# Kernel optimization log

Hardware: AMD Instinct MI355X
Metric: run time of the kernel (lower is better)

The kernel has to match this reference:

```python
import jax, jax.numpy as jnp
import numpy as np

B, S, D, H = 2, 2048, 1024, 16
HD = D // H
EPS = 1e-5


def layer_norm(x, g, b):
    m = jnp.mean(x, axis=-1, keepdims=True)
    v = jnp.mean(jnp.square(x - m), axis=-1, keepdims=True)
    return (x - m) * jax.lax.rsqrt(v + EPS) * g + b


def setup_inputs() -> dict:
    key = jax.random.key(0)
    ks = jax.random.split(key, 16)
    s = 0.02
    x = jax.random.normal(ks[0], (B, S, D), dtype=jnp.float32)
    mask = jax.random.randint(ks[1], (1, 1, S, S), 0, 2, dtype=jnp.int32)
    return {
        "x": x,
        "mask": mask,
        "Wq": jax.random.normal(ks[2], (D, D), jnp.float32) * s,
        "Wk": jax.random.normal(ks[3], (D, D), jnp.float32) * s,
        "Wv": jax.random.normal(ks[4], (D, D), jnp.float32) * s,
        "Wo": jax.random.normal(ks[5], (D, D), jnp.float32) * s,
        "bo": jax.random.normal(ks[6], (D,), jnp.float32) * s,
        "ln1_g": jnp.ones((D,), jnp.float32),
        "ln1_b": jnp.zeros((D,), jnp.float32),
        "W1": jax.random.normal(ks[7], (D, 4 * D), jnp.float32) * s,
        "b1": jax.random.normal(ks[8], (4 * D,), jnp.float32) * s,
        "W2": jax.random.normal(ks[9], (4 * D, D), jnp.float32) * s,
        "b2": jax.random.normal(ks[10], (D,), jnp.float32) * s,
        "ln2_g": jnp.ones((D,), jnp.float32),
        "ln2_b": jnp.zeros((D,), jnp.float32),
    }


def reference(x, mask, Wq, Wk, Wv, Wo, bo, ln1_g, ln1_b, W1, b1, W2, b2, ln2_g, ln2_b):
    # --- multi-head attention (dropout = identity in eval) ---
    q = (x @ Wq).reshape(B, S, H, HD)
    k = (x @ Wk).reshape(B, S, H, HD)
    v = (x @ Wv).reshape(B, S, H, HD)
    scores = jnp.einsum("bshd,bthd->bhst", q, k) / jnp.sqrt(jnp.float32(HD))
    scores = jnp.where(mask == 1, jnp.float32(-1e9), scores)
    p = jax.nn.softmax(scores, axis=-1)
    o = jnp.einsum("bhst,bthd->bshd", p, v).reshape(B, S, D)
    attn_out = o @ Wo + bo
    # --- residual with norm on the branch (note: norm applied to attn output) ---
    x = x + layer_norm(attn_out, ln1_g, ln1_b)
    # --- FFN: gelu after fc1 AND after fc2 (as in source) ---
    h = jax.nn.gelu(x @ W1 + b1, approximate=False)
    h = jax.nn.gelu(h @ W2 + b2, approximate=False)
    x = x + layer_norm(h, ln2_g, ln2_b)
    return x
```

## Files before the change

kernel.cpp:

```cpp
#include <hip/hip_runtime.h>
#include <hip/hip_bf16.h>
#include <cstdint>

#define BB 2
#define SS 2048
#define DD 1024
#define HH 16
#define HDIM 64
#define MROWS (BB*SS)

typedef __bf16 bf16;
using bf16x8 = __bf16 __attribute__((ext_vector_type(8)));
using bf16x4 = __bf16 __attribute__((ext_vector_type(4)));
using bf16x2 = __bf16 __attribute__((ext_vector_type(2)));
using f32x4  = float __attribute__((ext_vector_type(4)));

__device__ __forceinline__ float gelu_exact(float x) {
    return 0.5f * x * (1.f + erff(x * 0.70710678118654752f));
}

__device__ __forceinline__ void stage16(const bf16* g, bf16* lds_chunk_base, int lane) {
#if __has_builtin(__builtin_amdgcn_global_load_lds)
    __builtin_amdgcn_global_load_lds((const __attribute__((address_space(1))) void*)g,
                                     (__attribute__((address_space(3))) void*)lds_chunk_base,
                                     16, 0, 0);
#else
    *(bf16x8*)(lds_chunk_base + lane * 8) = *(const bf16x8*)g;
#endif
}

__global__ __launch_bounds__(256) void prep_kernel(
    const float* __restrict__ x, bf16* __restrict__ x_b,
    const int* __restrict__ mask, unsigned long long* __restrict__ maskb,
    const float* __restrict__ Wq, const float* __restrict__ Wk,
    const float* __restrict__ Wv, const float* __restrict__ Wo,
    const float* __restrict__ W1, const float* __restrict__ W2,
    bf16* __restrict__ Wqkv_t, bf16* __restrict__ Wo_t,
    bf16* __restrict__ W1_t, bf16* __restrict__ W2_t) {
    const int bid = blockIdx.x;
    if (bid < 4096) {
        int i = bid * 256 + threadIdx.x;
        float4 v = ((const float4*)x)[i];
        bf16x4 o;
        o[0] = (bf16)v.x; o[1] = (bf16)v.y; o[2] = (bf16)v.z; o[3] = (bf16)v.w;
        *(bf16x4*)(x_b + (size_t)i * 4) = o;
        return;
    }
    if (bid < 20480) {
        int gid = (bid - 4096) * 256 + threadIdx.x;
        int mv = mask[gid];
        unsigned long long bal = __ballot(mv == 1);
        if ((threadIdx.x & 63) == 0) maskb[gid >> 6] = bal;
        return;
    }
    int t = bid - 20480;
    const float* W; bf16* Wt; int K, N, bx, by;
    if (t < 4096) {
        int wsel = t >> 10;
        int tt = t & 1023;
        W  = (wsel == 0) ? Wq : (wsel == 1) ? Wk : (wsel == 2) ? Wv : Wo;
        Wt = (wsel == 3) ? Wo_t : (Wqkv_t + (size_t)wsel * 1024 * 1024);
        K = 1024; N = 1024; bx = (tt & 31) * 32; by = (tt >> 5) * 32;
    } else if (t < 8192) {
        int tt = t - 4096;
        W = W1; Wt = W1_t; K = 1024; N = 4096;
        bx = (tt & 127) * 32; by = (tt >> 7) * 32;
    } else {
        int tt = t - 8192;
        W = W2; Wt = W2_t; K = 4096; N = 1024;
        bx = (tt & 31) * 32; by = (tt >> 5) * 32;
    }
    __shared__ float tile[32][33];
    int tx = threadIdx.x & 31;
    int ty = threadIdx.x >> 5;
#pragma unroll
    for (int j = 0; j < 4; ++j)
        tile[ty + j * 8][tx] = W[(size_t)(by + ty + j * 8) * N + bx + tx];
    __syncthreads();
#pragma unroll
    for (int j = 0; j < 4; ++j)
        Wt[(size_t)(bx + ty + j * 8) * K + by + tx] = (bf16)tile[tx][ty + j * 8];
}

template <int EPI>
__global__ __launch_bounds__(256, 3) void gemm_bt(const bf16* __restrict__ A,
                                                  const bf16* __restrict__ Bt,
                                                  void* __restrict__ C,
                                                  void* __restrict__ C2,
                                                  const float* __restrict__ bias,
                                                  int M, int N, int K, int ldk) {
    __shared__ __align__(16) bf16 As[128 * 64];
    __shared__ __align__(16) bf16 Bs[128 * 64];
    const int tid  = threadIdx.x;
    const int lane = tid & 63;
    const int wave = tid >> 6;
    const int l16  = lane & 15;
    const int quad = lane >> 4;
    const int wm = wave >> 1, wn = wave & 1;
    const int m0 = blockIdx.y * 128, n0 = blockIdx.x * 128;
    const int z  = blockIdx.z;
    A  += (size_t)z * K;
    Bt += (size_t)z * K;

    f32x4 acc[4][4];
#pragma unroll
    for (int i = 0; i < 4; ++i)
#pragma unroll
        for (int j = 0; j < 4; ++j) acc[i][j] = (f32x4){0.f, 0.f, 0.f, 0.f};

    const int nsteps = K >> 6;
    for (int kt = 0; kt < nsteps; ++kt) {
        const int kbase = kt << 6;
#pragma unroll
        for (int c = 0; c < 4; ++c) {
            int chunk = wave * 4 + c;
            int gi = chunk * 64 + lane;
            int m  = gi >> 3;
            int cp = gi & 7;
            int g  = cp ^ (m & 7);
            stage16(A  + (size_t)(m0 + m) * ldk + kbase + g * 8, As + chunk * 512, lane);
            stage16(Bt + (size_t)(n0 + m) * ldk + kbase + g * 8, Bs + chunk * 512, lane);
        }
        __syncthreads();
#pragma unroll
        for (int ks = 0; ks < 2; ++ks) {
            bf16x8 af[4], bfr[4];
#pragma unroll
            for (int i = 0; i < 4; ++i) {
                int m = wm * 64 + i * 16 + l16;
                int g = ks * 4 + quad;
                af[i]  = *(const bf16x8*)(As + m * 64 + ((g ^ (m & 7)) * 8));
                int n = wn * 64 + i * 16 + l16;
                bfr[i] = *(const bf16x8*)(Bs + n * 64 + ((g ^ (n & 7)) * 8));
            }
#pragma unroll
            for (int i = 0; i < 4; ++i)
#pragma unroll
                for (int j = 0; j < 4; ++j)
                    acc[i][j] = __builtin_amdgcn_mfma_f32_16x16x32_bf16(af[i], bfr[j], acc[i][j], 0, 0, 0);
        }
        __syncthreads();
    }

    float* Cz = (EPI == 4) ? (z ? (float*)C2 : (float*)C) : nullptr;
#pragma unroll
    for (int i = 0; i < 4; ++i) {
        int row = m0 + wm * 64 + i * 16 + quad * 4;
#pragma unroll
        for (int j = 0; j < 4; ++j) {
            int col = n0 + wn * 64 + j * 16 + l16;
            float bv = (EPI == 2) ? bias[col] : 0.f;
#pragma unroll
            for (int r = 0; r < 4; ++r) {
                float v = acc[i][j][r];
                if (EPI == 2) v = gelu_exact(v + bv);
                size_t idx = (size_t)(row + r) * N + col;
                if (EPI == 4) Cz[idx] = v;
                else          ((bf16*)C)[idx] = (bf16)v;
            }
        }
    }
}

template <int EPI>
__global__ __launch_bounds__(512, 2) void gemm256(const bf16* __restrict__ A,
                                                  const bf16* __restrict__ Bt,
                                                  void* __restrict__ C0, void* __restrict__ C1,
                                                  void* __restrict__ C2v, void* __restrict__ C3,
                                                  const float* __restrict__ bias,
                                                  int M, int N, int K, int ldk) {
    __shared__ __align__(16) bf16 As[2 * 256 * 64];
    __shared__ __align__(16) bf16 Bs[2 * 256 * 64];
    const int tid  = threadIdx.x;
    const int lane = tid & 63;
    const int wave = tid >> 6;
    const int l16  = lane & 15;
    const int quad = lane >> 4;
    const int wm = wave >> 2;
    const int wn = wave & 3;
    const int m0 = blockIdx.y * 256, n0 = blockIdx.x * 256;
    const int z  = blockIdx.z;
    A  += (size_t)z * K;
    Bt += (size_t)z * K;

    const int rl = lane >> 3;
    const int cpn = lane & 7;
    const bf16* pA[4]; const bf16* pB[4];
    int ldsoff[4];
#pragma unroll
    for (int c = 0; c < 4; ++c) {
        int row = wave * 32 + c * 8 + rl;
        int g = cpn ^ (row & 7);
        pA[c] = A + (size_t)(m0 + row) * ldk + g * 8;
        pB[c] = Bt + (size_t)(n0 + row) * ldk + g * 8;
        ldsoff[c] = (wave * 4 + c) * 512;
    }

    f32x4 acc[8][4];
#pragma unroll
    for (int i = 0; i < 8; ++i)
#pragma unroll
        for (int j = 0; j < 4; ++j) acc[i][j] = (f32x4){0.f, 0.f, 0.f, 0.f};

    const int nt = K >> 6;

    auto stage_tile = [&](int t) {
        const int kb = t << 6;
        bf16* dstA = As + (t & 1) * 16384;
        bf16* dstB = Bs + (t & 1) * 16384;
#pragma unroll
        for (int c = 0; c < 4; ++c) stage16(pA[c] + kb, dstA + ldsoff[c], lane);
#pragma unroll
        for (int c = 0; c < 4; ++c) stage16(pB[c] + kb, dstB + ldsoff[c], lane);
    };

    stage_tile(0);
    stage_tile(1);
    asm volatile("s_waitcnt vmcnt(8)" ::: "memory");
    __builtin_amdgcn_s_barrier();

    for (int t = 0; t < nt; ++t) {
        const bf16* AsP = As + (t & 1) * 16384;
        const bf16* BsP = Bs + (t & 1) * 16384;
        bf16x8 af[4][2], b0[2][2], b1[2][2];

#pragma unroll
        for (int i = 0; i < 4; ++i) {
            int row = wm * 128 + i * 16 + l16;
#pragma unroll
            for (int kk = 0; kk < 2; ++kk)
                af[i][kk] = *(const bf16x8*)(AsP + row * 64 + (((kk * 4 + quad) ^ (row & 7)) * 8));
        }
#pragma unroll
        for (int j = 0; j < 2; ++j) {
            int row = wn * 64 + j * 16 + l16;
#pragma unroll
            for (int kk = 0; kk < 2; ++kk)
                b0[j][kk] = *(const bf16x8*)(BsP + row * 64 + (((kk * 4 + quad) ^ (row & 7)) * 8));
        }
        __builtin_amdgcn_s_barrier();
        __builtin_amdgcn_s_setprio(1);
#pragma unroll
        for (int i = 0; i < 4; ++i)
#pragma unroll
            for (int j = 0; j < 2; ++j)
#pragma unroll
                for (int kk = 0; kk < 2; ++kk)
                    acc[i][j] = __builtin_amdgcn_mfma_f32_16x16x32_bf16(af[i][kk], b0[j][kk], acc[i][j], 0, 0, 0);
        __builtin_amdgcn_s_setprio(0);
        __builtin_amdgcn_s_barrier();

#pragma unroll
        for (int j = 0; j < 2; ++j) {
            int row = wn * 64 + (j + 2) * 16 + l16;
#pragma unroll
            for (int kk = 0; kk < 2; ++kk)
                b1[j][kk] = *(const bf16x8*)(BsP + row * 64 + (((kk * 4 + quad) ^ (row & 7)) * 8));
        }
        __builtin_amdgcn_s_barrier();
        __builtin_amdgcn_s_setprio(1);
#pragma unroll
        for (int i = 0; i < 4; ++i)
#pragma unroll
            for (int j = 0; j < 2; ++j)
#pragma unroll
                for (int kk = 0; kk < 2; ++kk)
                    acc[i][j + 2] = __builtin_amdgcn_mfma_f32_16x16x32_bf16(af[i][kk], b1[j][kk], acc[i][j + 2], 0, 0, 0);
        __builtin_amdgcn_s_setprio(0);
        __builtin_amdgcn_s_barrier();

#pragma unroll
        for (int i = 0; i < 4; ++i) {
            int row = wm * 128 + 64 + i * 16 + l16;
#pragma unroll
            for (int kk = 0; kk < 2; ++kk)
                af[i][kk] = *(const bf16x8*)(AsP + row * 64 + (((kk * 4 + quad) ^ (row & 7)) * 8));
        }
        __builtin_amdgcn_s_barrier();
        __builtin_amdgcn_s_setprio(1);
#pragma unroll
        for (int i = 0; i < 4; ++i)
#pragma unroll
            for (int j = 0; j < 2; ++j)
#pragma unroll
                for (int kk = 0; kk < 2; ++kk)
                    acc[i + 4][j + 2] = __builtin_amdgcn_mfma_f32_16x16x32_bf16(af[i][kk], b1[j][kk], acc[i + 4][j + 2], 0, 0, 0);
        __builtin_amdgcn_s_setprio(0);
        __builtin_amdgcn_s_barrier();

        if (t + 2 < nt) stage_tile(t + 2);
        __builtin_amdgcn_s_barrier();
        __builtin_amdgcn_s_setprio(1);
#pragma unroll
        for (int i = 0; i < 4; ++i)
#pragma unroll
            for (int j = 0; j < 2; ++j)
#pragma unroll
                for (int kk = 0; kk < 2; ++kk)
                    acc[i + 4][j] = __builtin_amdgcn_mfma_f32_16x16x32_bf16(af[i][kk], b0[j][kk], acc[i + 4][j], 0, 0, 0);
        __builtin_amdgcn_s_setprio(0);
        if (t + 2 < nt) { asm volatile("s_waitcnt vmcnt(8)" ::: "memory"); }
        else            { asm volatile("s_waitcnt vmcnt(0)" ::: "memory"); }
        __builtin_amdgcn_s_barrier();
    }

    float* Cz = nullptr;
    if (EPI == 4) Cz = (z == 0) ? (float*)C0 : (z == 1) ? (float*)C1 : (z == 2) ? (float*)C2v : (float*)C3;
#pragma unroll
    for (int i = 0; i < 8; ++i) {
        int row = m0 + wm * 128 + i * 16 + quad * 4;
#pragma unroll
        for (int j = 0; j < 4; ++j) {
            int col = n0 + wn * 64 + j * 16 + l16;
            float bv = (EPI == 2) ? bias[col] : 0.f;
#pragma unroll
            for (int r = 0; r < 4; ++r) {
                float v = acc[i][j][r];
                if (EPI == 2) v = gelu_exact(v + bv);
                size_t idx = (size_t)(row + r) * N + col;
                if (EPI == 4) Cz[idx] = v;
                else          ((bf16*)C0)[idx] = (bf16)v;
            }
        }
    }
}

__global__ __launch_bounds__(512, 4) void flash_attn(const bf16* __restrict__ qkv,
                                                     const unsigned long long* __restrict__ maskb,
                                                     bf16* __restrict__ o) {
    __shared__ __align__(16) bf16 Ks[128 * 64];
    __shared__ __align__(16) bf16 Vts[64 * 136];
    const int tid  = threadIdx.x;
    const int lane = tid & 63;
    const int wave = tid >> 6;
    const int l16  = lane & 15;
    const int quad = lane >> 4;
    const int bh = blockIdx.y;
    const int b = bh >> 4, h = bh & 15;
    const int q0 = blockIdx.x * 128;
    const size_t rowb = (size_t)b * SS;
    const float SCL = 0.18033688011112042f;

    const size_t qrow = (rowb + q0 + wave * 16 + l16) * 3072 + h * 64;
    bf16x8 qf[2];
    {
        bf16x8 q0r = *(const bf16x8*)(qkv + qrow + quad * 8);
        bf16x8 q1r = *(const bf16x8*)(qkv + qrow + 32 + quad * 8);
#pragma unroll
        for (int j = 0; j < 8; ++j) {
            qf[0][j] = (bf16)((float)q0r[j] * SCL);
            qf[1][j] = (bf16)((float)q1r[j] * SCL);
        }
    }

    f32x4 oacc[4];
#pragma unroll
    for (int d = 0; d < 4; ++d) oacc[d] = (f32x4){0.f, 0.f, 0.f, 0.f};
    f32x4 lacc = (f32x4){0.f, 0.f, 0.f, 0.f};
    const int mrow32 = (q0 + wave * 16 + l16) * 32;

    bf16x8 ones;
#pragma unroll
    for (int j = 0; j < 8; ++j) ones[j] = (bf16)1.0f;

    const int vt_tc = (lane >> 4) * 32 + ((lane >> 1) & 3) * 8 + ((lane >> 3) & 1) * 4 + 2 * (lane & 1);
    const int vd8 = wave * 8;

    int kst[2], ksg[2];
#pragma unroll
    for (int c = 0; c < 2; ++c) {
        int gi = (wave * 2 + c) * 64 + lane;
        kst[c] = gi >> 3;
        ksg[c] = (gi & 7) ^ (kst[c] & 7);
    }

    bf16x8 kreg[2], vreg[2];
    ulonglong2 mwreg;
#pragma unroll
    for (int c = 0; c < 2; ++c)
        kreg[c] = *(const bf16x8*)(qkv + (rowb + kst[c]) * 3072 + 1024 + h * 64 + ksg[c] * 8);
    {
        const bf16* vg = qkv + (rowb + 2 * lane) * 3072 + 2048 + h * 64 + vd8;
        vreg[0] = *(const bf16x8*)(vg);
        vreg[1] = *(const bf16x8*)(vg + 3072);
    }
    mwreg = *(const ulonglong2*)(maskb + mrow32);

    for (int kt = 0; kt < SS / 128; ++kt) {
        __syncthreads();
#pragma unroll
        for (int c = 0; c < 2; ++c)
            *(bf16x8*)(Ks + (wave * 2 + c) * 512 + lane * 8) = kreg[c];
#pragma unroll
        for (int j = 0; j < 8; ++j) {
            bf16x2 pr; pr[0] = vreg[0][j]; pr[1] = vreg[1][j];
            *(bf16x2*)(Vts + (vd8 + j) * 136 + vt_tc) = pr;
        }
        ulonglong2 mw = mwreg;
        __syncthreads();

        if (kt + 1 < SS / 128) {
            const int t0n = (kt + 1) * 128;
#pragma unroll
            for (int c = 0; c < 2; ++c)
                kreg[c] = *(const bf16x8*)(qkv + (rowb + t0n + kst[c]) * 3072 + 1024 + h * 64 + ksg[c] * 8);
            {
                const bf16* vg = qkv + (rowb + t0n + 2 * lane) * 3072 + 2048 + h * 64 + vd8;
                vreg[0] = *(const bf16x8*)(vg);
                vreg[1] = *(const bf16x8*)(vg + 3072);
            }
            mwreg = *(const ulonglong2*)(maskb + mrow32 + (kt + 1) * 2);
        }

        f32x4 st[8];
        __builtin_amdgcn_s_setprio(1);
#pragma unroll
        for (int tg = 0; tg < 8; ++tg) {
            int tl = tg * 16 + l16;
            bf16x8 a0 = *(const bf16x8*)(Ks + tl * 64 + ((quad       ^ (tl & 7)) * 8));
            bf16x8 a1 = *(const bf16x8*)(Ks + tl * 64 + (((4 + quad) ^ (tl & 7)) * 8));
            f32x4 s = (f32x4){0.f, 0.f, 0.f, 0.f};
            s = __builtin_amdgcn_mfma_f32_16x16x32_bf16(a0, qf[0], s, 0, 0, 0);
            s = __builtin_amdgcn_mfma_f32_16x16x32_bf16(a1, qf[1], s, 0, 0, 0);
            st[tg] = s;
        }
        __builtin_amdgcn_s_setprio(0);

        unsigned long long s0 = mw.x >> (quad * 4);
        unsigned long long s1 = mw.y >> (quad * 4);
        bf16x8 pva[4];
#pragma unroll
        for (int tg = 0; tg < 8; ++tg) {
            unsigned int bits = (unsigned int)(((tg < 4) ? s0 : s1) >> ((tg & 3) * 16));
#pragma unroll
            for (int r = 0; r < 4; ++r) {
                float p = __builtin_amdgcn_exp2f(st[tg][r]);
                p = ((bits >> r) & 1u) ? 0.f : p;
                pva[tg >> 1][(tg & 1) * 4 + r] = (bf16)p;
            }
        }

        __builtin_amdgcn_s_setprio(1);
#pragma unroll
        for (int kc = 0; kc < 4; ++kc) {
#pragma unroll
            for (int dg = 0; dg < 4; ++dg) {
                bf16x8 bfrag = *(const bf16x8*)(Vts + (dg * 16 + l16) * 136 + kc * 32 + quad * 8);
                oacc[dg] = __builtin_amdgcn_mfma_f32_16x16x32_bf16(pva[kc], bfrag, oacc[dg], 0, 0, 0);
            }
            lacc = __builtin_amdgcn_mfma_f32_16x16x32_bf16(pva[kc], ones, lacc, 0, 0, 0);
        }
        __builtin_amdgcn_s_setprio(0);
    }

#pragma unroll
    for (int r = 0; r < 4; ++r) {
        float inv_l = 1.f / lacc[r];
        bf16* orow = o + (rowb + q0 + wave * 16 + quad * 4 + r) * DD + h * 64;
#pragma unroll
        for (int dg = 0; dg < 4; ++dg)
            orow[dg * 16 + l16] = (bf16)(oacc[dg][r] * inv_l);
    }
}

template <bool GELU, bool WB16, int NP>
__global__ __launch_bounds__(256) void ln_fused(const float* __restrict__ resid,
                                                const float* __restrict__ p0,
                                                const float* __restrict__ p1,
                                                const float* __restrict__ p2,
                                                const float* __restrict__ p3,
                                                const float* __restrict__ bias,
                                                const float* __restrict__ g,
                                                const float* __restrict__ bb,
                                                float* __restrict__ outf,
                                                bf16* __restrict__ outb) {
    const int row = blockIdx.x;
    const int tid = threadIdx.x;
    const size_t base = (size_t)row * DD + tid * 4;
    float4 a0 = *(const float4*)(p0 + base);
    float4 a1 = *(const float4*)(p1 + base);
    float4 bz = *(const float4*)(bias + tid * 4);
    float ax = a0.x + a1.x + bz.x;
    float ay = a0.y + a1.y + bz.y;
    float az = a0.z + a1.z + bz.z;
    float aw = a0.w + a1.w + bz.w;
    if (NP == 4) {
        float4 a2 = *(const float4*)(p2 + base);
        float4 a3 = *(const float4*)(p3 + base);
        ax += a2.x + a3.x; ay += a2.y + a3.y; az += a2.z + a3.z; aw += a2.w + a3.w;
    }
    if (GELU) { ax = gelu_exact(ax); ay = gelu_exact(ay); az = gelu_exact(az); aw = gelu_exact(aw); }
    float s1 = ax + ay + az + aw;
    float s2 = ax * ax + ay * ay + az * az + aw * aw;
#pragma unroll
    for (int off = 32; off; off >>= 1) {
        s1 += __shfl_xor(s1, off, 64);
        s2 += __shfl_xor(s2, off, 64);
    }
    __shared__ float red[8];
    if ((tid & 63) == 0) { red[(tid >> 6) * 2] = s1; red[(tid >> 6) * 2 + 1] = s2; }
    __syncthreads();
    s1 = red[0] + red[2] + red[4] + red[6];
    s2 = red[1] + red[3] + red[5] + red[7];
    float mean = s1 * (1.f / DD);
    float var  = s2 * (1.f / DD) - mean * mean;
    float rs = rsqrtf(var + 1e-5f);
    float4 gv = *(const float4*)(g + tid * 4);
    float4 bv = *(const float4*)(bb + tid * 4);
    float4 rv = *(const float4*)(resid + base);
    float y0 = rv.x + (ax - mean) * rs * gv.x + bv.x;
    float y1 = rv.y + (ay - mean) * rs * gv.y + bv.y;
    float y2 = rv.z + (az - mean) * rs * gv.z + bv.z;
    float y3 = rv.w + (aw - mean) * rs * gv.w + bv.w;
    float4 yo = make_float4(y0, y1, y2, y3);
    *(float4*)(outf + base) = yo;
    if (WB16) {
        bf16x4 ob;
        ob[0] = (bf16)y0; ob[1] = (bf16)y1; ob[2] = (bf16)y2; ob[3] = (bf16)y3;
        *(bf16x4*)(outb + base) = ob;
    }
}

extern "C" void kernel_launch(void* const* d_in, const int* in_sizes, int n_in,
                              void* d_out, int out_size, void* d_ws, size_t ws_size,
                              hipStream_t stream) {
    const float* x    = (const float*)d_in[0];
    const int*   mask = (const int*)d_in[1];
    const float* Wq   = (const float*)d_in[2];
    const float* Wk   = (const float*)d_in[3];
    const float* Wv   = (const float*)d_in[4];
    const float* Wo   = (const float*)d_in[5];
    const float* bo   = (const float*)d_in[6];
    const float* ln1g = (const float*)d_in[7];
    const float* ln1b = (const float*)d_in[8];
    const float* W1   = (const float*)d_in[9];
    const float* b1   = (const float*)d_in[10];
    const float* W2   = (const float*)d_in[11];
    const float* b2   = (const float*)d_in[12];
    const float* ln2g = (const float*)d_in[13];
    const float* ln2b = (const float*)d_in[14];

    char* w = (char*)d_ws;
    bf16* Wqkv_t = (bf16*)w; w += (size_t)3072 * 1024 * 2;
    bf16* Wo_t   = (bf16*)w; w += (size_t)1024 * 1024 * 2;
    bf16* W1_t   = (bf16*)w; w += (size_t)4096 * 1024 * 2;
    bf16* W2_t   = (bf16*)w; w += (size_t)1024 * 4096 * 2;
    bf16* x_b    = (bf16*)w; w += (size_t)MROWS * DD * 2;
    bf16* qkv    = (bf16*)w; w += (size_t)MROWS * 3072 * 2;
    float* R     = (float*)w; w += (size_t)MROWS * DD * 8;
    float* x1_f  = (float*)w; w += (size_t)MROWS * DD * 4;
    unsigned long long* maskb = (unsigned long long*)w; w += (size_t)SS * 32 * 8;
    bf16* o_b  = x_b;
    bf16* x1_b = x_b;
    float* op0 = R;
    float* op1 = R + (size_t)MROWS * DD;
    bf16*  h_b = (bf16*)R;
    float* fp0 = (float*)d_out;
    float* fp1 = (float*)x_b;
    float* fp2 = (float*)x_b + (size_t)4 * 1024 * 1024;
    float* fp3 = (float*)d_ws;

    prep_kernel<<<32768, 256, 0, stream>>>(x, x_b, mask, maskb,
                                           Wq, Wk, Wv, Wo, W1, W2,
                                           Wqkv_t, Wo_t, W1_t, W2_t);

    gemm256<0><<<dim3(12, 16, 1), 512, 0, stream>>>(x_b, Wqkv_t, qkv, nullptr, nullptr, nullptr, nullptr, MROWS, 3072, 1024, 1024);
    flash_attn<<<dim3(SS / 128, BB * HH), 512, 0, stream>>>(qkv, maskb, o_b);
    gemm_bt<4><<<dim3(8, 32, 2), 256, 0, stream>>>(o_b, Wo_t, op0, op1, nullptr, MROWS, 1024, 512, 1024);
    ln_fused<false, true, 2><<<MROWS, 256, 0, stream>>>(x, op0, op1, nullptr, nullptr, bo, ln1g, ln1b, x1_f, x1_b);
    gemm256<2><<<dim3(16, 16, 1), 512, 0, stream>>>(x1_b, W1_t, h_b, nullptr, nullptr, nullptr, b1, MROWS, 4096, 1024, 1024);
    gemm256<4><<<dim3(4, 16, 4), 512, 0, stream>>>(h_b, W2_t, fp0, fp1, fp2, fp3, nullptr, MROWS, 1024, 1024, 4096);
    ln_fused<true, false, 4><<<MROWS, 256, 0, stream>>>(x1_f, fp0, fp1, fp2, fp3, b2, ln2g, ln2b, (float*)d_out, nullptr);
}
```

Before: 438.0 us.

## Remap workgroups across XCDs and interleave gemm256 staging with MFMA phases

Adds a workgroup index remap in both GEMM kernels and the flash attention kernel so that consecutive logical tiles land on the same XCD, improving L2 locality. In gemm256, global-to-LDS staging is split into half-tile chunks issued between the MFMA phases instead of in one burst. LDS fragment reads now go through inline-asm ds_read_b128 with precomputed swizzled addresses, with explicit lgkmcnt waits and sched barriers. This spreads memory traffic across the compute loop, but the manual waitcnt bookkeeping and the dropped memory clobbers risk ordering bugs and stalls.

```diff
diff --git a/kernel.cpp b/kernel.cpp
--- a/kernel.cpp
+++ b/kernel.cpp
@@ -27,6 +27,16 @@
 #else
     *(bf16x8*)(lds_chunk_base + lane * 8) = *(const bf16x8*)g;
 #endif
+}
+
+__device__ __forceinline__ unsigned lds_addr(const void* p) {
+    return (unsigned)(uintptr_t)(const __attribute__((address_space(3))) void*)p;
+}
+
+__device__ __forceinline__ bf16x8 dsr(unsigned addr) {
+    bf16x8 r;
+    asm volatile("ds_read_b128 %0, %1" : "=v"(r) : "v"(addr));
+    return r;
 }
 
 __global__ __launch_bounds__(256) void prep_kernel(
@@ -97,8 +107,20 @@
     const int l16  = lane & 15;
     const int quad = lane >> 4;
     const int wm = wave >> 1, wn = wave & 1;
-    const int m0 = blockIdx.y * 128, n0 = blockIdx.x * 128;
-    const int z  = blockIdx.z;
+
+    int bx, by, bz;
+    {
+        const int Gx = gridDim.x, Gy = gridDim.y, Gz = gridDim.z;
+        const int nwg = Gx * Gy * Gz;
+        int L = blockIdx.x + Gx * (blockIdx.y + Gy * blockIdx.z);
+        if ((nwg & 7) == 0) {
+            int chunk = nwg >> 3;
+            L = (L & 7) * chunk + (L >> 3);
+        }
+        bx = L % Gx; int rest = L / Gx; by = rest % Gy; bz = rest / Gy;
+    }
+    const int m0 = by * 128, n0 = bx * 128;
+    const int z  = bz;
     A  += (size_t)z * K;
     Bt += (size_t)z * K;
 
@@ -169,8 +191,8 @@
                                                   void* __restrict__ C2v, void* __restrict__ C3,
                                                   const float* __restrict__ bias,
                                                   int M, int N, int K, int ldk) {
-    __shared__ __align__(16) bf16 As[2 * 256 * 64];
-    __shared__ __align__(16) bf16 Bs[2 * 256 * 64];
+    __shared__ __align__(16) bf16 As[2 * 16384];
+    __shared__ __align__(16) bf16 Bs[2 * 16384];
     const int tid  = threadIdx.x;
     const int lane = tid & 63;
     const int wave = tid >> 6;
@@ -178,23 +200,35 @@
     const int quad = lane >> 4;
     const int wm = wave >> 2;
     const int wn = wave & 3;
-    const int m0 = blockIdx.y * 256, n0 = blockIdx.x * 256;
-    const int z  = blockIdx.z;
+
+    int bx, by, bz;
+    {
+        const int Gx = gridDim.x, Gy = gridDim.y, Gz = gridDim.z;
+        const int nwg = Gx * Gy * Gz;
+        int L = blockIdx.x + Gx * (blockIdx.y + Gy * blockIdx.z);
+        if ((nwg & 7) == 0) {
+            int chunk = nwg >> 3;
+            L = (L & 7) * chunk + (L >> 3);
+        }
+        bx = L % Gx; int rest = L / Gx; by = rest % Gy; bz = rest / Gy;
+    }
+    const int m0 = by * 256, n0 = bx * 256;
+    const int z  = bz;
     A  += (size_t)z * K;
     Bt += (size_t)z * K;
 
-    const int rl = lane >> 3;
-    const int cpn = lane & 7;
-    const bf16* pA[4]; const bf16* pB[4];
-    int ldsoff[4];
-#pragma unroll
-    for (int c = 0; c < 4; ++c) {
-        int row = wave * 32 + c * 8 + rl;
-        int g = cpn ^ (row & 7);
-        pA[c] = A + (size_t)(m0 + row) * ldk + g * 8;
-        pB[c] = Bt + (size_t)(n0 + row) * ldk + g * 8;
-        ldsoff[c] = (wave * 4 + c) * 512;
-    }
+    const int grow = wave * 8 + (lane >> 3);
+    const int gg   = (lane & 7) ^ (grow & 7);
+    const bf16* sA = A  + (size_t)(m0 + grow) * ldk + gg * 8;
+    const bf16* sB = Bt + (size_t)(n0 + grow) * ldk + gg * 8;
+    const int dchunk = wave * 512;
+
+    const unsigned s7 = (unsigned)(l16 & 7);
+    const unsigned e0 = ((unsigned)quad ^ s7) * 16;
+    const unsigned arow0 = (unsigned)(wm * 128 + l16) * 128;
+    const unsigned brow0 = (unsigned)(wn * 64 + l16) * 128;
+    const unsigned asBase = lds_addr(As);
+    const unsigned bsBase = lds_addr(Bs);
 
     f32x4 acc[8][4];
 #pragma unroll
@@ -204,41 +238,43 @@
 
     const int nt = K >> 6;
 
-    auto stage_tile = [&](int t) {
+    auto stageHalf = [&](int t, int R0, bool isB) {
         const int kb = t << 6;
-        bf16* dstA = As + (t & 1) * 16384;
-        bf16* dstB = Bs + (t & 1) * 16384;
-#pragma unroll
-        for (int c = 0; c < 4; ++c) stage16(pA[c] + kb, dstA + ldsoff[c], lane);
-#pragma unroll
-        for (int c = 0; c < 4; ++c) stage16(pB[c] + kb, dstB + ldsoff[c], lane);
+        const bf16* s = isB ? sB : sA;
+        bf16* d = (isB ? Bs : As) + (t & 1) * 16384 + R0 * 64 + dchunk;
+        stage16(s + (size_t)R0 * ldk + kb, d, lane);
+        stage16(s + (size_t)(R0 + 64) * ldk + kb, d + 4096, lane);
     };
 
-    stage_tile(0);
-    stage_tile(1);
-    asm volatile("s_waitcnt vmcnt(8)" ::: "memory");
+    stageHalf(0, 0, false); stageHalf(0, 128, false);
+    stageHalf(0, 0, true);  stageHalf(0, 128, true);
+    if (1 < nt) {
+        stageHalf(1, 0, false);
+        asm volatile("s_waitcnt vmcnt(2)");
+    } else {
+        asm volatile("s_waitcnt vmcnt(0)");
+    }
     __builtin_amdgcn_s_barrier();
 
     for (int t = 0; t < nt; ++t) {
-        const bf16* AsP = As + (t & 1) * 16384;
-        const bf16* BsP = Bs + (t & 1) * 16384;
+        const unsigned ab = asBase + (unsigned)(t & 1) * 32768 + arow0;
+        const unsigned bb = bsBase + (unsigned)(t & 1) * 32768 + brow0;
         bf16x8 af[4][2], b0[2][2], b1[2][2];
 
 #pragma unroll
         for (int i = 0; i < 4; ++i) {
-            int row = wm * 128 + i * 16 + l16;
-#pragma unroll
-            for (int kk = 0; kk < 2; ++kk)
-                af[i][kk] = *(const bf16x8*)(AsP + row * 64 + (((kk * 4 + quad) ^ (row & 7)) * 8));
+            af[i][0] = dsr(ab + i * 2048 + e0);
+            af[i][1] = dsr(ab + i * 2048 + (e0 ^ 64));
         }
 #pragma unroll
         for (int j = 0; j < 2; ++j) {
-            int row = wn * 64 + j * 16 + l16;
-#pragma unroll
-            for (int kk = 0; kk < 2; ++kk)
-                b0[j][kk] = *(const bf16x8*)(BsP + row * 64 + (((kk * 4 + quad) ^ (row & 7)) * 8));
-        }
-        __builtin_amdgcn_s_barrier();
+            b0[j][0] = dsr(bb + j * 2048 + e0);
+            b0[j][1] = dsr(bb + j * 2048 + (e0 ^ 64));
+        }
+        if (t + 1 < nt) { stageHalf(t + 1, 128, false); stageHalf(t + 1, 0, true); }
+        __builtin_amdgcn_s_barrier();
+        asm volatile("s_waitcnt lgkmcnt(0)");
+        __builtin_amdgcn_sched_barrier(0);
         __builtin_amdgcn_s_setprio(1);
 #pragma unroll
         for (int i = 0; i < 4; ++i)
@@ -252,12 +288,13 @@
 
 #pragma unroll
         for (int j = 0; j < 2; ++j) {
-            int row = wn * 64 + (j + 2) * 16 + l16;
-#pragma unroll
-            for (int kk = 0; kk < 2; ++kk)
-                b1[j][kk] = *(const bf16x8*)(BsP + row * 64 + (((kk * 4 + quad) ^ (row & 7)) * 8));
-        }
-        __builtin_amdgcn_s_barrier();
+            b1[j][0] = dsr(bb + 4096 + j * 2048 + e0);
+            b1[j][1] = dsr(bb + 4096 + j * 2048 + (e0 ^ 64));
+        }
+        if (t + 1 < nt) stageHalf(t + 1, 128, true);
+        __builtin_amdgcn_s_barrier();
+        asm volatile("s_waitcnt lgkmcnt(0)");
+        __builtin_amdgcn_sched_barrier(0);
         __builtin_amdgcn_s_setprio(1);
 #pragma unroll
         for (int i = 0; i < 4; ++i)
@@ -271,12 +308,12 @@
 
 #pragma unroll
         for (int i = 0; i < 4; ++i) {
-            int row = wm * 128 + 64 + i * 16 + l16;
-#pragma unroll
-            for (int kk = 0; kk < 2; ++kk)
-                af[i][kk] = *(const bf16x8*)(AsP + row * 64 + (((kk * 4 + quad) ^ (row & 7)) * 8));
-        }
-        __builtin_amdgcn_s_barrier();
+            af[i][0] = dsr(ab + 8192 + i * 2048 + e0);
+            af[i][1] = dsr(ab + 8192 + i * 2048 + (e0 ^ 64));
+        }
+        __builtin_amdgcn_s_barrier();
+        asm volatile("s_waitcnt lgkmcnt(0)");
+        __builtin_amdgcn_sched_barrier(0);
         __builtin_amdgcn_s_setprio(1);
 #pragma unroll
         for (int i = 0; i < 4; ++i)
@@ -288,7 +325,7 @@
         __builtin_amdgcn_s_setprio(0);
         __builtin_amdgcn_s_barrier();
 
-        if (t + 2 < nt) stage_tile(t + 2);
+        if (t + 2 < nt) stageHalf(t + 2, 0, false);
         __builtin_amdgcn_s_barrier();
         __builtin_amdgcn_s_setprio(1);
 #pragma unroll
@@ -299,8 +336,8 @@
                 for (int kk = 0; kk < 2; ++kk)
                     acc[i + 4][j] = __builtin_amdgcn_mfma_f32_16x16x32_bf16(af[i][kk], b0[j][kk], acc[i + 4][j], 0, 0, 0);
         __builtin_amdgcn_s_setprio(0);
-        if (t + 2 < nt) { asm volatile("s_waitcnt vmcnt(8)" ::: "memory"); }
-        else            { asm volatile("s_waitcnt vmcnt(0)" ::: "memory"); }
+        if (t + 2 < nt) { asm volatile("s_waitcnt vmcnt(2)"); }
+        else            { asm volatile("s_waitcnt vmcnt(0)"); }
         __builtin_amdgcn_s_barrier();
     }
 
@@ -335,9 +372,18 @@
     const int wave = tid >> 6;
     const int l16  = lane & 15;
     const int quad = lane >> 4;
-    const int bh = blockIdx.y;
+
+    int bqx, bhy;
+    {
+        const int Gx = gridDim.x, Gy = gridDim.y;
+        int L = blockIdx.x + Gx * blockIdx.y;
+        int chunk = (Gx * Gy) >> 3;
+        L = (L & 7) * chunk + (L >> 3);
+        bqx = L % Gx; bhy = L / Gx;
+    }
+    const int bh = bhy;
     const int b = bh >> 4, h = bh & 15;
-    const int q0 = blockIdx.x * 128;
+    const int q0 = bqx * 128;
     const size_t rowb = (size_t)b * SS;
     const float SCL = 0.18033688011112042f;
 
```

Result: faster. 371.9 us (-15.1%).
